# Kernel tuning notes

Hardware: AMD Instinct MI355X
Metric: run time of the kernel (lower is better)

Reference implementation:

```python
import jax, jax.numpy as jnp
import numpy as np

NEG_FILL = -1000.0

def setup_inputs() -> dict:
    key = jax.random.key(0)
    k1, k2, k3, k4 = jax.random.split(key, 4)
    B, N, D = 16, 2048, 64
    q = jax.random.normal(k1, (B, N, D), dtype=jnp.float32)
    k = jax.random.normal(k2, (B, N, D), dtype=jnp.float32)
    v = jax.random.normal(k3, (B, N, D), dtype=jnp.float32)
    mask = jax.random.randint(k4, (B, N, N), 0, 2) == 1
    return {"q": q, "k": k, "v": v, "mask": mask}

def reference(q, k, v, mask):
    # Faithful to the torch module: scale by sqrt(seq_len) = len(q[0])**0.5,
    # masked positions set to -1000.0, softmax over dim=1 (NOT the last dim).
    seq_len = q.shape[1]
    scores = jnp.einsum('bnd,bmd->bnm', q, k) / jnp.sqrt(jnp.float32(seq_len))
    scores = jnp.where(mask, NEG_FILL, scores)
    attn = jax.nn.softmax(scores, axis=1)  # dim=1 as in nn.Softmax(dim=1)
    out = jnp.einsum('bnm,bmd->bnd', attn, v)
    return out
```

## Files before the change

### kernel.cpp

```cpp
#include <hip/hip_runtime.h>
#include <hip/hip_bf16.h>


#define B_ 16
#define N_ 2048
#define D_ 64
#define SCALE 0.022097086912079608f
#define NCH 8

typedef __attribute__((ext_vector_type(8))) short bf16x8;
typedef __attribute__((ext_vector_type(4))) float f32x4;
typedef unsigned char u8;

static __device__ __forceinline__ short f2bf(float x) {
  unsigned u = __float_as_uint(x);
  return (short)((u + 0x7FFF + ((u >> 16) & 1)) >> 16);
}

static __device__ __forceinline__ bf16x8 load8(const short* p) {
  return *reinterpret_cast<const bf16x8*>(p);
}

static __device__ __forceinline__ bf16x8 load8f(const float* p) {
  const f32x4 a = *reinterpret_cast<const f32x4*>(p);
  const f32x4 b = *reinterpret_cast<const f32x4*>(p + 4);
  bf16x8 r;
  r[0] = f2bf(a[0]); r[1] = f2bf(a[1]); r[2] = f2bf(a[2]); r[3] = f2bf(a[3]);
  r[4] = f2bf(b[0]); r[5] = f2bf(b[1]); r[6] = f2bf(b[2]); r[7] = f2bf(b[3]);
  return r;
}

__global__ __launch_bounds__(256) void cvt_bf16(const float* __restrict__ q,
                                                const float* __restrict__ k,
                                                short* __restrict__ qb,
                                                short* __restrict__ kb) {
  const size_t i = ((size_t)blockIdx.x * 256 + threadIdx.x) * 8;
  const float* src = blockIdx.y ? k : q;
  short* dst = blockIdx.y ? kb : qb;
  *reinterpret_cast<bf16x8*>(dst + i) = load8f(src + i);
}

__global__ __launch_bounds__(256) void cspack_kernel(
    const short* __restrict__ qb, const short* __restrict__ kb,
    const int* __restrict__ mask, u8* __restrict__ pk,
    float* __restrict__ csp) {
  const int b = blockIdx.x;
  const int wave = threadIdx.x >> 6;
  const int lane = threadIdx.x & 63;
  const int l15 = lane & 15;
  const int lhi = lane >> 4;
  const int m0 = blockIdx.y * 128 + wave * 32;
  const int mi = m0 >> 5;
  const int nbase = blockIdx.z * (N_ / NCH);

  const short* qbb = qb + (size_t)b * N_ * D_;
  const short* kbb = kb + (size_t)b * N_ * D_;
  const int* maskb = mask + (size_t)b * N_ * N_;

  bf16x8 kf[2][2];
#pragma unroll
  for (int cg = 0; cg < 2; ++cg) {
    kf[cg][0] = load8(kbb + (m0 + cg * 16 + l15) * D_ + lhi * 8);
    kf[cg][1] = load8(kbb + (m0 + cg * 16 + l15) * D_ + 32 + lhi * 8);
  }

  float cs0 = 0.f, cs1 = 0.f;

  for (int n0 = nbase; n0 < nbase + N_ / NCH; n0 += 16) {
    int mk[2][4];
#pragma unroll
    for (int cg = 0; cg < 2; ++cg)
#pragma unroll
      for (int r = 0; r < 4; ++r)
        mk[cg][r] =
            maskb[(size_t)(n0 + lhi * 4 + r) * N_ + m0 + cg * 16 + l15];
    const bf16x8 qf0 = load8(qbb + (n0 + l15) * D_ + lhi * 8);
    const bf16x8 qf1 = load8(qbb + (n0 + l15) * D_ + 32 + lhi * 8);
    unsigned pbyte = 0;
#pragma unroll
    for (int cg = 0; cg < 2; ++cg) {
      f32x4 acc = {0.f, 0.f, 0.f, 0.f};
      acc = __builtin_amdgcn_mfma_f32_16x16x32_bf16(qf0, kf[cg][0], acc, 0, 0, 0);
      acc = __builtin_amdgcn_mfma_f32_16x16x32_bf16(qf1, kf[cg][1], acc, 0, 0, 0);
      float cp = 0.f;
#pragma unroll
      for (int r = 0; r < 4; ++r) {
        const float p = mk[cg][r] ? 0.f : __expf(acc[r] * SCALE);
        cp += p;
        pbyte |= (mk[cg][r] ? 1u : 0u) << (cg * 4 + r);
      }
      if (cg == 0) cs0 += cp; else cs1 += cp;
    }
    const int n16 = n0 >> 4;
    pk[(((size_t)b * 128 + n16) * 64 + mi) * 64 + lane] = (u8)pbyte;
  }

  cs0 += __shfl_xor(cs0, 16, 64);
  cs0 += __shfl_xor(cs0, 32, 64);
  cs1 += __shfl_xor(cs1, 16, 64);
  cs1 += __shfl_xor(cs1, 32, 64);
  float* cspz = csp + ((size_t)b * NCH + blockIdx.z) * N_;
  if (lane < 16) {
    cspz[m0 + l15] = cs0;
    cspz[m0 + 16 + l15] = cs1;
  }
}

__global__ __launch_bounds__(256) void vprep_kernel(
    const float* __restrict__ v, const float* __restrict__ csp,
    short* __restrict__ vt) {
  const int b = blockIdx.x;
  const int m0 = blockIdx.y * 64;
  const int tid = threadIdx.x;
  __shared__ float csl[4][64];
  __shared__ float cst[64];
  __shared__ float lds[64][65];

  {
    const int col = m0 + (tid & 63);
    const int q4 = tid >> 6;
    float s = 0.f;
#pragma unroll
    for (int j = 0; j < 2; ++j)
      s += csp[((size_t)b * NCH + q4 * 2 + j) * N_ + col];
    csl[q4][tid & 63] = s;
  }
  __syncthreads();
  if (tid < 64) cst[tid] = csl[0][tid] + csl[1][tid] + csl[2][tid] + csl[3][tid];
  __syncthreads();

  const float* vb = v + (size_t)b * N_ * D_;
#pragma unroll
  for (int pass = 0; pass < 4; ++pass) {
    const int mloc = pass * 16 + (tid >> 4);
    const int d4 = (tid & 15) * 4;
    const f32x4 x = *reinterpret_cast<const f32x4*>(vb + (m0 + mloc) * D_ + d4);
    const float ic = 1.0f / cst[mloc];
    lds[mloc][d4 + 0] = x[0] * ic;
    lds[mloc][d4 + 1] = x[1] * ic;
    lds[mloc][d4 + 2] = x[2] * ic;
    lds[mloc][d4 + 3] = x[3] * ic;
  }
  __syncthreads();
  const int d = tid >> 2;
  const int seg = tid & 3;
  bf16x8 o0, o1;
#pragma unroll
  for (int i = 0; i < 8; ++i) o0[i] = f2bf(lds[seg * 16 + i][d]);
#pragma unroll
  for (int i = 0; i < 8; ++i) o1[i] = f2bf(lds[seg * 16 + 8 + i][d]);
  short* dst = vt + (size_t)b * D_ * N_ + (size_t)d * N_ + m0 + seg * 16;
  *reinterpret_cast<bf16x8*>(dst) = o0;
  *reinterpret_cast<bf16x8*>(dst + 8) = o1;
}

__global__ __launch_bounds__(256) void out2_kernel(
    const short* __restrict__ qb, const short* __restrict__ kb,
    const u8* __restrict__ pk, const short* __restrict__ vt,
    float* __restrict__ out) {
  const int b = blockIdx.x;
  const int wave = threadIdx.x >> 6;
  const int lane = threadIdx.x & 63;
  const int l15 = lane & 15;
  const int lhi = lane >> 4;
  const int n16 = blockIdx.y * 4 + wave;
  const int n0 = n16 * 16;

  const short* qbb = qb + (size_t)b * N_ * D_;
  const short* kbb = kb + (size_t)b * N_ * D_;
  const short* vtb = vt + (size_t)b * D_ * N_;

  const bf16x8 qf0 = load8(qbb + (n0 + l15) * D_ + lhi * 8);
  const bf16x8 qf1 = load8(qbb + (n0 + l15) * D_ + 32 + lhi * 8);

  __shared__ __align__(16) u8 pks[4][4096];
  __shared__ __align__(16) short pbuf[4][16][40];
  {
    const f32x4* src = reinterpret_cast<const f32x4*>(
        pk + ((size_t)b * 128 + n16) * 4096);
    f32x4* dst = reinterpret_cast<f32x4*>(pks[wave]);
#pragma unroll
    for (int j = 0; j < 4; ++j) dst[j * 64 + lane] = src[j * 64 + lane];
  }

  f32x4 oacc[4];
#pragma unroll
  for (int d = 0; d < 4; ++d) oacc[d] = (f32x4){0.f, 0.f, 0.f, 0.f};

#pragma unroll 2
  for (int mi = 0; mi < 64; ++mi) {
    const int m0 = mi * 32;
    const unsigned pbyte = pks[wave][mi * 64 + lane];
#pragma unroll
    for (int cg = 0; cg < 2; ++cg) {
      const bf16x8 kf0 = load8(kbb + (m0 + cg * 16 + l15) * D_ + lhi * 8);
      const bf16x8 kf1 = load8(kbb + (m0 + cg * 16 + l15) * D_ + 32 + lhi * 8);
      f32x4 acc = {0.f, 0.f, 0.f, 0.f};
      acc = __builtin_amdgcn_mfma_f32_16x16x32_bf16(qf0, kf0, acc, 0, 0, 0);
      acc = __builtin_amdgcn_mfma_f32_16x16x32_bf16(qf1, kf1, acc, 0, 0, 0);
#pragma unroll
      for (int r = 0; r < 4; ++r) {
        const float p = ((pbyte >> (cg * 4 + r)) & 1u)
                            ? 0.f
                            : __expf(acc[r] * SCALE);
        pbuf[wave][lhi * 4 + r][cg * 16 + l15] = f2bf(p);
      }
    }
    const bf16x8 pa =
        *reinterpret_cast<const bf16x8*>(&pbuf[wave][l15][lhi * 8]);
#pragma unroll
    for (int dsub = 0; dsub < 4; ++dsub) {
      const bf16x8 vf =
          load8(vtb + (size_t)(dsub * 16 + l15) * N_ + m0 + lhi * 8);
      oacc[dsub] =
          __builtin_amdgcn_mfma_f32_16x16x32_bf16(pa, vf, oacc[dsub], 0, 0, 0);
    }
  }

  float* dst = out + (size_t)b * N_ * D_;
#pragma unroll
  for (int dsub = 0; dsub < 4; ++dsub)
#pragma unroll
    for (int r = 0; r < 4; ++r)
      dst[(size_t)(n0 + lhi * 4 + r) * D_ + dsub * 16 + l15] = oacc[dsub][r];
}

__global__ __launch_bounds__(256) void colsum_fb(
    const float* __restrict__ q, const float* __restrict__ k,
    const int* __restrict__ mask, float* __restrict__ colsum) {
  const int b = blockIdx.x;
  const int wave = threadIdx.x >> 6;
  const int lane = threadIdx.x & 63;
  const int l15 = lane & 15;
  const int lhi = lane >> 4;
  const int m0 = blockIdx.y * 64 + wave * 16;
  const float* qbp = q + (size_t)b * N_ * D_;
  const float* kbp = k + (size_t)b * N_ * D_;
  const int* maskb = mask + (size_t)b * N_ * N_;
  const bf16x8 kf0 = load8f(kbp + (m0 + l15) * D_ + lhi * 8);
  const bf16x8 kf1 = load8f(kbp + (m0 + l15) * D_ + 32 + lhi * 8);
  float partial = 0.f;
  for (int n0 = 0; n0 < N_; n0 += 16) {
    bf16x8 qf0 = load8f(qbp + (n0 + l15) * D_ + lhi * 8);
    bf16x8 qf1 = load8f(qbp + (n0 + l15) * D_ + 32 + lhi * 8);
    f32x4 acc = {0.f, 0.f, 0.f, 0.f};
    acc = __builtin_amdgcn_mfma_f32_16x16x32_bf16(qf0, kf0, acc, 0, 0, 0);
    acc = __builtin_amdgcn_mfma_f32_16x16x32_bf16(qf1, kf1, acc, 0, 0, 0);
#pragma unroll
    for (int r = 0; r < 4; ++r) {
      const int n = n0 + lhi * 4 + r;
      partial +=
          maskb[(size_t)n * N_ + m0 + l15] ? 0.f : __expf(acc[r] * SCALE);
    }
  }
  partial += __shfl_xor(partial, 16, 64);
  partial += __shfl_xor(partial, 32, 64);
  if (lane < 16) colsum[(size_t)b * N_ + m0 + l15] = partial;
}

__global__ __launch_bounds__(256) void attn_out_fb(
    const float* __restrict__ q, const float* __restrict__ k,
    const float* __restrict__ v, const int* __restrict__ mask,
    const float* __restrict__ colsum, float* __restrict__ out) {
  const int b = blockIdx.x;
  const int wave = threadIdx.x >> 6;
  const int lane = threadIdx.x & 63;
  const int l15 = lane & 15;
  const int lhi = lane >> 4;
  const int n0 = blockIdx.y * 64 + wave * 16;
  const float* qbp = q + (size_t)b * N_ * D_;
  const float* kbp = k + (size_t)b * N_ * D_;
  const float* vbp = v + (size_t)b * N_ * D_;
  const int* maskb = mask + (size_t)b * N_ * N_;
  const float* csb = colsum + (size_t)b * N_;
  const bf16x8 qf0 = load8f(qbp + (n0 + l15) * D_ + lhi * 8);
  const bf16x8 qf1 = load8f(qbp + (n0 + l15) * D_ + 32 + lhi * 8);
  __shared__ __align__(16) short pbuf[4][16][32];
  f32x4 oacc[4];
#pragma unroll
  for (int d = 0; d < 4; ++d) oacc[d] = (f32x4){0.f, 0.f, 0.f, 0.f};
  for (int m0 = 0; m0 < N_; m0 += 32) {
#pragma unroll
    for (int cg = 0; cg < 2; ++cg) {
      const int mc = m0 + cg * 16;
      bf16x8 kf0 = load8f(kbp + (mc + l15) * D_ + lhi * 8);
      bf16x8 kf1 = load8f(kbp + (mc + l15) * D_ + 32 + lhi * 8);
      f32x4 acc = {0.f, 0.f, 0.f, 0.f};
      acc = __builtin_amdgcn_mfma_f32_16x16x32_bf16(qf0, kf0, acc, 0, 0, 0);
      acc = __builtin_amdgcn_mfma_f32_16x16x32_bf16(qf1, kf1, acc, 0, 0, 0);
      const float ic = 1.0f / csb[mc + l15];
#pragma unroll
      for (int r = 0; r < 4; ++r) {
        const int n = n0 + lhi * 4 + r;
        const float p = maskb[(size_t)n * N_ + mc + l15]
                            ? 0.f
                            : __expf(acc[r] * SCALE) * ic;
        pbuf[wave][lhi * 4 + r][cg * 16 + l15] = f2bf(p);
      }
    }
    __syncthreads();
    const bf16x8 pa =
        *reinterpret_cast<const bf16x8*>(&pbuf[wave][l15][lhi * 8]);
#pragma unroll
    for (int dsub = 0; dsub < 4; ++dsub) {
      bf16x8 vf;
#pragma unroll
      for (int j = 0; j < 8; ++j)
        vf[j] = f2bf(vbp[(m0 + lhi * 8 + j) * D_ + dsub * 16 + l15]);
      oacc[dsub] =
          __builtin_amdgcn_mfma_f32_16x16x32_bf16(pa, vf, oacc[dsub], 0, 0, 0);
    }
    __syncthreads();
  }
#pragma unroll
  for (int dsub = 0; dsub < 4; ++dsub)
#pragma unroll
    for (int r = 0; r < 4; ++r)
      out[(size_t)b * N_ * D_ + (size_t)(n0 + lhi * 4 + r) * D_ + dsub * 16 +
          l15] = oacc[dsub][r];
}

extern "C" void kernel_launch(void* const* d_in, const int* in_sizes, int n_in,
                              void* d_out, int out_size, void* d_ws,
                              size_t ws_size, hipStream_t stream) {
  const float* q = (const float*)d_in[0];
  const float* k = (const float*)d_in[1];
  const float* v = (const float*)d_in[2];
  const int* mask = (const int*)d_in[3];
  float* out = (float*)d_out;

  const size_t MB = 1024 * 1024;
  const size_t qb_off = 0;
  const size_t kb_off = qb_off + 4 * MB;
  const size_t vt_off = kb_off + 4 * MB;
  const size_t cs_off = vt_off + 4 * MB;
  const size_t pk_off = cs_off + 1 * MB;
  const size_t need = pk_off + 8 * MB;

  if (ws_size >= need) {
    short* qbf = (short*)((char*)d_ws + qb_off);
    short* kbf = (short*)((char*)d_ws + kb_off);
    short* vt = (short*)((char*)d_ws + vt_off);
    float* csp = (float*)((char*)d_ws + cs_off);
    u8* pk = (u8*)((char*)d_ws + pk_off);

    cvt_bf16<<<dim3((B_ * N_ * D_) / (256 * 8), 2), 256, 0, stream>>>(
        q, k, qbf, kbf);
    cspack_kernel<<<dim3(B_, N_ / 128, NCH), 256, 0, stream>>>(qbf, kbf, mask,
                                                               pk, csp);
    vprep_kernel<<<dim3(B_, N_ / 64), 256, 0, stream>>>(v, csp, vt);
    out2_kernel<<<dim3(B_, N_ / 64), 256, 0, stream>>>(qbf, kbf, pk, vt, out);
  } else {
    float* colsum = (float*)d_ws;
    colsum_fb<<<dim3(B_, N_ / 64), 256, 0, stream>>>(q, k, mask, colsum);
    attn_out_fb<<<dim3(B_, N_ / 64), 256, 0, stream>>>(q, k, v, mask, colsum,
                                                       out);
  }
}
```

Baseline: 498.4 us.

## Split output kernel over key dimension and reduce partial results

Splits out2_kernel's loop over key blocks into two halves along a new grid z dimension, so twice as many blocks run. Each half writes fp32 partial outputs to workspace, and a new reduce kernel sums them. The loop also alternates between two LDS P buffers so consecutive steps do not share one buffer. The price is an extra kernel launch, 16 MB of partial-output traffic and a larger workspace requirement; if the workspace is too small, execution falls back to the slower path.

```diff
diff --git a/kernel.cpp b/kernel.cpp
--- a/kernel.cpp
+++ b/kernel.cpp
@@ -7,6 +7,7 @@
 #define D_ 64
 #define SCALE 0.022097086912079608f
 #define NCH 8
+#define MSPLIT 2
 
 typedef __attribute__((ext_vector_type(8))) short bf16x8;
 typedef __attribute__((ext_vector_type(4))) float f32x4;
@@ -154,10 +155,37 @@
   *reinterpret_cast<bf16x8*>(dst + 8) = o1;
 }
 
+#define OSTEP(MI, PB)                                                          \
+  {                                                                            \
+    const int m0s = (miBase + (MI)) * 32;                                      \
+    const unsigned pbyte = pks[wave][(MI) * 64 + lane];                        \
+    _Pragma("unroll") for (int cg = 0; cg < 2; ++cg) {                         \
+      const bf16x8 kf0 = load8(kbb + (m0s + cg * 16 + l15) * D_ + lhi * 8);    \
+      const bf16x8 kf1 =                                                       \
+          load8(kbb + (m0s + cg * 16 + l15) * D_ + 32 + lhi * 8);              \
+      f32x4 acc = {0.f, 0.f, 0.f, 0.f};                                        \
+      acc = __builtin_amdgcn_mfma_f32_16x16x32_bf16(qf0, kf0, acc, 0, 0, 0);   \
+      acc = __builtin_amdgcn_mfma_f32_16x16x32_bf16(qf1, kf1, acc, 0, 0, 0);   \
+      _Pragma("unroll") for (int r = 0; r < 4; ++r) {                          \
+        const float p =                                                        \
+            ((pbyte >> (cg * 4 + r)) & 1u) ? 0.f : __expf(acc[r] * SCALE);     \
+        PB[wave][lhi * 4 + r][cg * 16 + l15] = f2bf(p);                        \
+      }                                                                        \
+    }                                                                          \
+    const bf16x8 pa =                                                          \
+        *reinterpret_cast<const bf16x8*>(&PB[wave][l15][lhi * 8]);             \
+    _Pragma("unroll") for (int dsub = 0; dsub < 4; ++dsub) {                   \
+      const bf16x8 vf =                                                        \
+          load8(vtb + (size_t)(dsub * 16 + l15) * N_ + m0s + lhi * 8);         \
+      oacc[dsub] =                                                             \
+          __builtin_amdgcn_mfma_f32_16x16x32_bf16(pa, vf, oacc[dsub], 0, 0, 0);\
+    }                                                                          \
+  }
+
 __global__ __launch_bounds__(256) void out2_kernel(
     const short* __restrict__ qb, const short* __restrict__ kb,
     const u8* __restrict__ pk, const short* __restrict__ vt,
-    float* __restrict__ out) {
+    float* __restrict__ outp) {
   const int b = blockIdx.x;
   const int wave = threadIdx.x >> 6;
   const int lane = threadIdx.x & 63;
@@ -165,6 +193,7 @@
   const int lhi = lane >> 4;
   const int n16 = blockIdx.y * 4 + wave;
   const int n0 = n16 * 16;
+  const int miBase = blockIdx.z * (64 / MSPLIT);
 
   const short* qbb = qb + (size_t)b * N_ * D_;
   const short* kbb = kb + (size_t)b * N_ * D_;
@@ -173,56 +202,44 @@
   const bf16x8 qf0 = load8(qbb + (n0 + l15) * D_ + lhi * 8);
   const bf16x8 qf1 = load8(qbb + (n0 + l15) * D_ + 32 + lhi * 8);
 
-  __shared__ __align__(16) u8 pks[4][4096];
-  __shared__ __align__(16) short pbuf[4][16][40];
+  __shared__ __align__(16) u8 pks[4][2048];
+  __shared__ __align__(16) short pbA[4][16][40];
+  __shared__ __align__(16) short pbB[4][16][40];
   {
     const f32x4* src = reinterpret_cast<const f32x4*>(
-        pk + ((size_t)b * 128 + n16) * 4096);
+        pk + (((size_t)b * 128 + n16) * 64 + miBase) * 64);
     f32x4* dst = reinterpret_cast<f32x4*>(pks[wave]);
 #pragma unroll
-    for (int j = 0; j < 4; ++j) dst[j * 64 + lane] = src[j * 64 + lane];
+    for (int j = 0; j < 2; ++j) dst[j * 64 + lane] = src[j * 64 + lane];
   }
 
   f32x4 oacc[4];
 #pragma unroll
   for (int d = 0; d < 4; ++d) oacc[d] = (f32x4){0.f, 0.f, 0.f, 0.f};
 
-#pragma unroll 2
-  for (int mi = 0; mi < 64; ++mi) {
-    const int m0 = mi * 32;
-    const unsigned pbyte = pks[wave][mi * 64 + lane];
-#pragma unroll
-    for (int cg = 0; cg < 2; ++cg) {
-      const bf16x8 kf0 = load8(kbb + (m0 + cg * 16 + l15) * D_ + lhi * 8);
-      const bf16x8 kf1 = load8(kbb + (m0 + cg * 16 + l15) * D_ + 32 + lhi * 8);
-      f32x4 acc = {0.f, 0.f, 0.f, 0.f};
-      acc = __builtin_amdgcn_mfma_f32_16x16x32_bf16(qf0, kf0, acc, 0, 0, 0);
-      acc = __builtin_amdgcn_mfma_f32_16x16x32_bf16(qf1, kf1, acc, 0, 0, 0);
-#pragma unroll
-      for (int r = 0; r < 4; ++r) {
-        const float p = ((pbyte >> (cg * 4 + r)) & 1u)
-                            ? 0.f
-                            : __expf(acc[r] * SCALE);
-        pbuf[wave][lhi * 4 + r][cg * 16 + l15] = f2bf(p);
-      }
-    }
-    const bf16x8 pa =
-        *reinterpret_cast<const bf16x8*>(&pbuf[wave][l15][lhi * 8]);
-#pragma unroll
-    for (int dsub = 0; dsub < 4; ++dsub) {
-      const bf16x8 vf =
-          load8(vtb + (size_t)(dsub * 16 + l15) * N_ + m0 + lhi * 8);
-      oacc[dsub] =
-          __builtin_amdgcn_mfma_f32_16x16x32_bf16(pa, vf, oacc[dsub], 0, 0, 0);
-    }
-  }
-
-  float* dst = out + (size_t)b * N_ * D_;
+  for (int mi2 = 0; mi2 < 64 / MSPLIT; mi2 += 2) {
+    OSTEP(mi2, pbA);
+    OSTEP(mi2 + 1, pbB);
+  }
+
+  float* dst = outp + ((size_t)blockIdx.z * B_ + b) * N_ * D_;
 #pragma unroll
   for (int dsub = 0; dsub < 4; ++dsub)
 #pragma unroll
     for (int r = 0; r < 4; ++r)
       dst[(size_t)(n0 + lhi * 4 + r) * D_ + dsub * 16 + l15] = oacc[dsub][r];
+}
+
+__global__ __launch_bounds__(256) void reduce2_kernel(
+    const float* __restrict__ outp, float* __restrict__ out) {
+  const size_t i = ((size_t)blockIdx.x * 256 + threadIdx.x) * 4;
+  const f32x4 a = *reinterpret_cast<const f32x4*>(outp + i);
+  const f32x4 c =
+      *reinterpret_cast<const f32x4*>(outp + (size_t)B_ * N_ * D_ + i);
+  f32x4 r;
+  r[0] = a[0] + c[0]; r[1] = a[1] + c[1];
+  r[2] = a[2] + c[2]; r[3] = a[3] + c[3];
+  *reinterpret_cast<f32x4*>(out + i) = r;
 }
 
 __global__ __launch_bounds__(256) void colsum_fb(
@@ -335,7 +352,8 @@
   const size_t vt_off = kb_off + 4 * MB;
   const size_t cs_off = vt_off + 4 * MB;
   const size_t pk_off = cs_off + 1 * MB;
-  const size_t need = pk_off + 8 * MB;
+  const size_t op_off = pk_off + 8 * MB;
+  const size_t need = op_off + 16 * MB;
 
   if (ws_size >= need) {
     short* qbf = (short*)((char*)d_ws + qb_off);
@@ -343,13 +361,17 @@
     short* vt = (short*)((char*)d_ws + vt_off);
     float* csp = (float*)((char*)d_ws + cs_off);
     u8* pk = (u8*)((char*)d_ws + pk_off);
+    float* outp = (float*)((char*)d_ws + op_off);
 
     cvt_bf16<<<dim3((B_ * N_ * D_) / (256 * 8), 2), 256, 0, stream>>>(
         q, k, qbf, kbf);
     cspack_kernel<<<dim3(B_, N_ / 128, NCH), 256, 0, stream>>>(qbf, kbf, mask,
                                                                pk, csp);
     vprep_kernel<<<dim3(B_, N_ / 64), 256, 0, stream>>>(v, csp, vt);
-    out2_kernel<<<dim3(B_, N_ / 64), 256, 0, stream>>>(qbf, kbf, pk, vt, out);
+    out2_kernel<<<dim3(B_, N_ / 64, MSPLIT), 256, 0, stream>>>(qbf, kbf, pk,
+                                                               vt, outp);
+    reduce2_kernel<<<dim3((B_ * N_ * D_) / (256 * 4)), 256, 0, stream>>>(outp,
+                                                                         out);
   } else {
     float* colsum = (float*)d_ws;
     colsum_fb<<<dim3(B_, N_ / 64), 256, 0, stream>>>(q, k, mask, colsum);
```

Measured after the change: 506.8 us. No clear change (+1.7%).
